# Kernel optimization log

Measured on AMD Instinct MI355X. Metric: run time of the kernel, lower is better.

Reference implementation:

```python
import jax, jax.numpy as jnp
import numpy as np

B, T, C = 2, 2048, 2048
H, HK = 16, 4
HD = C // H
N_REP = H // HK


def setup_inputs() -> dict:
    key = jax.random.key(0)
    ks = jax.random.split(key, 10)
    sc_in = 1.0 / np.sqrt(C)
    x = jax.random.normal(ks[0], (B, T, C), dtype=jnp.float32)
    # rotary embeddings (realistic cos/sin from inv_freq)
    inv_freq = 1.0 / (10000.0 ** (jnp.arange(0, HD, 2, dtype=jnp.float32) / HD))
    freqs = jnp.arange(T, dtype=jnp.float32)[:, None] * inv_freq[None, :]  # [T, HD/2]
    emb = jnp.concatenate([freqs, freqs], axis=-1)  # [T, HD]
    cos = jnp.broadcast_to(jnp.cos(emb)[None], (B, T, HD))
    sin = jnp.broadcast_to(jnp.sin(emb)[None], (B, T, HD))
    Wq = jax.random.normal(ks[1], (C, H * HD), dtype=jnp.float32) * sc_in
    bq = jnp.zeros((H * HD,), dtype=jnp.float32)
    Wk = jax.random.normal(ks[2], (C, HK * HD), dtype=jnp.float32) * sc_in
    bk = jnp.zeros((HK * HD,), dtype=jnp.float32)
    Wv = jax.random.normal(ks[3], (C, HK * HD), dtype=jnp.float32) * sc_in
    bv = jnp.zeros((HK * HD,), dtype=jnp.float32)
    Wo = jax.random.normal(ks[4], (C, C), dtype=jnp.float32) * sc_in
    return {"x": x, "cos": cos, "sin": sin, "Wq": Wq, "bq": bq,
            "Wk": Wk, "bk": bk, "Wv": Wv, "bv": bv, "Wo": Wo}


def _rotate_half(t):
    t1, t2 = jnp.split(t, 2, axis=-1)
    return jnp.concatenate([-t2, t1], axis=-1)


def reference(x, cos, sin, Wq, bq, Wk, bk, Wv, bv, Wo):
    b, t, c = x.shape
    q = (x @ Wq + bq).reshape(b, t, H, HD).transpose(0, 2, 1, 3)   # [B,H,T,HD]
    k = (x @ Wk + bk).reshape(b, t, HK, HD).transpose(0, 2, 1, 3)  # [B,HK,T,HD]
    v = (x @ Wv + bv).reshape(b, t, HK, HD).transpose(0, 2, 1, 3)  # [B,HK,T,HD]
    co = cos[:, None, :, :]  # [B,1,T,HD]
    si = sin[:, None, :, :]
    q = q * co + _rotate_half(q) * si
    k = k * co + _rotate_half(k) * si
    # GQA without materializing repeated K/V: group query heads per KV head
    qg = q.reshape(b, HK, N_REP, t, HD)
    scale = 1.0 / np.sqrt(HD)
    scores = jnp.einsum('bgrqd,bgkd->bgrqk', qg, k) * scale  # [B,HK,n_rep,T,T]
    causal = jnp.tril(jnp.ones((t, t), dtype=bool))
    scores = jnp.where(causal, scores, jnp.finfo(scores.dtype).min)
    att = jax.nn.softmax(scores, axis=-1)
    yg = jnp.einsum('bgrqk,bgkd->bgrqd', att, v)  # [B,HK,n_rep,T,HD]
    y = yg.reshape(b, H, t, HD).transpose(0, 2, 1, 3).reshape(b, t, c)
    return y @ Wo
```

## Files before the change

kernel.cpp:

```cpp
#include <hip/hip_runtime.h>
#include <math.h>

#define BB 2
#define TT 2048
#define CC 2048
#define HH 16
#define HKK 4
#define HD 128
#define MM (BB*TT)

typedef short bf16x8 __attribute__((ext_vector_type(8)));
typedef float f32x4 __attribute__((ext_vector_type(4)));

#define GLOBAL_AS(p) ((const __attribute__((address_space(1))) void*)(p))
#define LDS_AS(p)    ((__attribute__((address_space(3))) void*)(p))

__device__ __forceinline__ unsigned short f2bf(float f) {
    unsigned u = __float_as_uint(f);
    u += 0x7fff + ((u >> 16) & 1);
    return (unsigned short)(u >> 16);
}
__device__ __forceinline__ float bf2f(unsigned short h) {
    return __uint_as_float(((unsigned)h) << 16);
}

#define QSCALE (0.08838834764831845f * 1.44269504088896340736f)

__global__ __launch_bounds__(256) void cast_x_kernel(
    const float* __restrict__ x, unsigned short* __restrict__ xb)
{
    size_t i = ((size_t)blockIdx.x * 256 + threadIdx.x) * 8;
    float4 a = *(const float4*)&x[i];
    float4 b = *(const float4*)&x[i + 4];
    uint4 r;
    r.x = f2bf(a.x) | ((unsigned)f2bf(a.y) << 16);
    r.y = f2bf(a.z) | ((unsigned)f2bf(a.w) << 16);
    r.z = f2bf(b.x) | ((unsigned)f2bf(b.y) << 16);
    r.w = f2bf(b.z) | ((unsigned)f2bf(b.w) << 16);
    *(uint4*)&xb[i] = r;
}

__global__ __launch_bounds__(256) void wtrans_kernel(
    const float* __restrict__ Wq, const float* __restrict__ Wk,
    const float* __restrict__ Wv, const float* __restrict__ Wo,
    unsigned short* __restrict__ Wt, unsigned short* __restrict__ Wot)
{
    __shared__ float tile[64][65];
    int z = blockIdx.z;
    const float* src; unsigned short* dst; int ldW, nmax, noff;
    if (z == 0)      { src = Wq; dst = Wt;  ldW = 2048; nmax = 2048; noff = 0; }
    else if (z == 1) { src = Wk; dst = Wt;  ldW = 512;  nmax = 512;  noff = 2048; }
    else if (z == 2) { src = Wv; dst = Wt;  ldW = 512;  nmax = 512;  noff = 2560; }
    else             { src = Wo; dst = Wot; ldW = 2048; nmax = 2048; noff = 0; }
    int n0 = blockIdx.y * 64;
    if (n0 >= nmax) return;
    int k0 = blockIdx.x * 64;
    int tx = threadIdx.x & 15, ty = threadIdx.x >> 4;
#pragma unroll
    for (int i = 0; i < 4; ++i) {
        int r = ty + i * 16;
        float4 v4 = *(const float4*)&src[(size_t)(k0 + r) * ldW + n0 + tx * 4];
        tile[r][tx * 4 + 0] = v4.x;
        tile[r][tx * 4 + 1] = v4.y;
        tile[r][tx * 4 + 2] = v4.z;
        tile[r][tx * 4 + 3] = v4.w;
    }
    __syncthreads();
#pragma unroll
    for (int i = 0; i < 4; ++i) {
        int r = ty + i * 16;
        int c = tx * 4;
        ushort4 o;
        o.x = f2bf(tile[c + 0][r]);
        o.y = f2bf(tile[c + 1][r]);
        o.z = f2bf(tile[c + 2][r]);
        o.w = f2bf(tile[c + 3][r]);
        *(ushort4*)&dst[(size_t)(noff + n0 + r) * 2048 + k0 + c] = o;
    }
}

__device__ __forceinline__ void gemm_core_128x128x64(
    const unsigned short* __restrict__ A, const unsigned short* __restrict__ B,
    short* As, short* Bs, int m0, int n0,
    const int* mrow, const int* nrow, f32x4 (&acc)[4][4])
{
    const int tid = threadIdx.x;
    const int lane = tid & 63;
    const int w = tid >> 6;
    const int lm = lane & 15;
    const int q8 = lane >> 4;
    const int lrow = lane >> 3;
    const int lchunk = lane & 7;

    for (int kt = 0; kt < CC; kt += 64) {
        __syncthreads();
#pragma unroll
        for (int jj = 0; jj < 4; ++jj) {
            int rA = w * 32 + jj * 8 + lrow;
            int cA = ((lchunk ^ (rA & 7)) << 3);
            __builtin_amdgcn_global_load_lds(
                GLOBAL_AS(&A[(size_t)(m0 + rA) * CC + kt + cA]),
                LDS_AS(&As[(w * 32 + jj * 8) * 64]), 16, 0, 0);
            __builtin_amdgcn_global_load_lds(
                GLOBAL_AS(&B[(size_t)(n0 + rA) * CC + kt + cA]),
                LDS_AS(&Bs[(w * 32 + jj * 8) * 64]), 16, 0, 0);
        }
        __syncthreads();
#pragma unroll
        for (int ksi = 0; ksi < 2; ++ksi) {
            bf16x8 af[4], bfr[4];
#pragma unroll
            for (int i = 0; i < 4; ++i) {
                int xo = (((ksi * 4 + q8) ^ (lm & 7)) << 3);
                af[i]  = *(const bf16x8*)&As[(mrow[i] + lm) * 64 + xo];
                bfr[i] = *(const bf16x8*)&Bs[(nrow[i] + lm) * 64 + xo];
            }
#pragma unroll
            for (int im = 0; im < 4; ++im)
#pragma unroll
                for (int in = 0; in < 4; ++in)
                    acc[im][in] = __builtin_amdgcn_mfma_f32_16x16x32_bf16(af[im], bfr[in], acc[im][in], 0, 0, 0);
        }
    }
}

__global__ __launch_bounds__(256, 3) void qkv_gemm_mfma(
    const unsigned short* __restrict__ xb, const unsigned short* __restrict__ Wt,
    const float* __restrict__ bq, const float* __restrict__ bk, const float* __restrict__ bv,
    const float* __restrict__ cosb, const float* __restrict__ sinb,
    unsigned short* __restrict__ q, unsigned short* __restrict__ k, unsigned short* __restrict__ v)
{
    __shared__ __attribute__((aligned(16))) short As[128 * 64];
    __shared__ __attribute__((aligned(16))) short Bs[128 * 64];
    const int lane = threadIdx.x & 63;
    const int w = threadIdx.x >> 6;
    const int w1 = w >> 1;
    const int m0 = blockIdx.y * 128;
    const int n0 = blockIdx.x * 128;
    const int lm = lane & 15;
    const int q8 = lane >> 4;

    int mrow[4], nrow[4];
#pragma unroll
    for (int i = 0; i < 4; ++i) {
        mrow[i] = (w & 1) * 64 + i * 16;
        nrow[i] = w1 * 32 + (i & 1) * 16 + (i >> 1) * 64;
    }

    f32x4 acc[4][4];
#pragma unroll
    for (int im = 0; im < 4; ++im)
#pragma unroll
        for (int in = 0; in < 4; ++in) acc[im][in] = {0.f, 0.f, 0.f, 0.f};

    gemm_core_128x128x64(xb, Wt, As, Bs, m0, n0, mrow, nrow, acc);

    unsigned short* dst; const float* bias; int ldD, off, mode;
    if (n0 < 2048)      { dst = q; bias = bq; ldD = 2048; off = n0;        mode = 0; }
    else if (n0 < 2560) { dst = k; bias = bk; ldD = 512;  off = n0 - 2048; mode = 1; }
    else                { dst = v; bias = bv; ldD = 512;  off = n0 - 2560; mode = 2; }

    float bv_[4];
#pragma unroll
    for (int in = 0; in < 4; ++in) bv_[in] = bias[off + nrow[in] + lm];

#pragma unroll
    for (int im = 0; im < 4; ++im) {
        int rowbase = m0 + mrow[im] + q8 * 4;
        float t[4][4];
#pragma unroll
        for (int in = 0; in < 4; ++in)
#pragma unroll
            for (int r = 0; r < 4; ++r) t[in][r] = acc[im][in][r] + bv_[in];
        if (mode < 2) {
#pragma unroll
            for (int in = 0; in < 4; ++in) {
                int d = nrow[in] + lm;
                float sgn = (in < 2) ? -1.f : 1.f;
#pragma unroll
                for (int r = 0; r < 4; ++r) {
                    int row = rowbase + r;
                    float c = cosb[row * HD + d];
                    float s = sinb[row * HD + d];
                    float o = c * t[in][r] + sgn * s * t[in ^ 2][r];
                    if (mode == 0) o *= QSCALE;
                    dst[(size_t)row * ldD + off + d] = f2bf(o);
                }
            }
        } else {
#pragma unroll
            for (int in = 0; in < 4; ++in)
#pragma unroll
                for (int r = 0; r < 4; ++r)
                    dst[(size_t)(rowbase + r) * ldD + off + nrow[in] + lm] = f2bf(t[in][r]);
        }
    }
}

__global__ __launch_bounds__(256, 3) void out_gemm_mfma(
    const unsigned short* __restrict__ yb, const unsigned short* __restrict__ Wot,
    float* __restrict__ Cout)
{
    __shared__ __attribute__((aligned(16))) short As[128 * 64];
    __shared__ __attribute__((aligned(16))) short Bs[128 * 64];
    const int lane = threadIdx.x & 63;
    const int w = threadIdx.x >> 6;
    const int m0 = blockIdx.y * 128;
    const int n0 = blockIdx.x * 128;
    const int lm = lane & 15;
    const int q8 = lane >> 4;

    int mrow[4], nrow[4];
#pragma unroll
    for (int i = 0; i < 4; ++i) {
        mrow[i] = (w & 1) * 64 + i * 16;
        nrow[i] = (w >> 1) * 64 + i * 16;
    }

    f32x4 acc[4][4];
#pragma unroll
    for (int im = 0; im < 4; ++im)
#pragma unroll
        for (int in = 0; in < 4; ++in) acc[im][in] = {0.f, 0.f, 0.f, 0.f};

    gemm_core_128x128x64(yb, Wot, As, Bs, m0, n0, mrow, nrow, acc);

#pragma unroll
    for (int im = 0; im < 4; ++im)
#pragma unroll
        for (int in = 0; in < 4; ++in)
#pragma unroll
            for (int r = 0; r < 4; ++r) {
                int row = m0 + mrow[im] + q8 * 4 + r;
                Cout[(size_t)row * CC + n0 + nrow[in] + lm] = acc[im][in][r];
            }
}

__global__ __launch_bounds__(256) void vtrans_kernel(
    const unsigned short* __restrict__ v, unsigned short* __restrict__ vt)
{
    __shared__ unsigned short tile[64][68];
    int bg = blockIdx.z;
    int b = bg >> 2, g = bg & 3;
    int t0 = blockIdx.x * 64;
    int d0 = blockIdx.y * 64;
    int tx = threadIdx.x & 15, ty = threadIdx.x >> 4;
#pragma unroll
    for (int i = 0; i < 4; ++i) {
        int r = ty + i * 16;
        ushort4 v4 = *(const ushort4*)&v[(size_t)(b * TT + t0 + r) * (HKK * HD) + g * HD + d0 + tx * 4];
        tile[r][tx * 4 + 0] = v4.x;
        tile[r][tx * 4 + 1] = v4.y;
        tile[r][tx * 4 + 2] = v4.z;
        tile[r][tx * 4 + 3] = v4.w;
    }
    __syncthreads();
#pragma unroll
    for (int i = 0; i < 4; ++i) {
        int r = ty + i * 16;
        int c = tx * 4;
        ushort4 o;
        o.x = tile[c + 0][r];
        o.y = tile[c + 1][r];
        o.z = tile[c + 2][r];
        o.w = tile[c + 3][r];
        *(ushort4*)&vt[(size_t)(bg * HD + d0 + r) * TT + t0 + c] = o;
    }
}

__global__ __launch_bounds__(512, 4) void flash_mfma(
    const unsigned short* __restrict__ q, const unsigned short* __restrict__ k,
    const unsigned short* __restrict__ vt, unsigned short* __restrict__ y)
{
    __shared__ __attribute__((aligned(16))) short SM[27136];
    short* Ks = SM;
    short* Vs = SM + 8704;
    short* Ps = SM + 17920;

    const int tid = threadIdx.x;
    const int lane = tid & 63;
    const int w = tid >> 6;
    const int lm = lane & 15;
    const int q8 = lane >> 4;
    const int bh = blockIdx.x;
    const int b = bh >> 4, h = bh & 15, g = h >> 2;
    const int yb_ = blockIdx.y;
    const int qi = (yb_ < 8) ? (15 - yb_) : (yb_ - 8);
    const int q0 = qi * 128;
    const int wrow = w * 16;
    const int jdiag = 2 * qi + (w >> 2);
    const int jmax = 2 * qi + 1;

    bf16x8 qf[4];
#pragma unroll
    for (int ks = 0; ks < 4; ++ks)
        qf[ks] = *(const bf16x8*)&q[(size_t)(b * TT + q0 + wrow + lm) * CC
                                    + h * HD + ks * 32 + q8 * 8];

    f32x4 o_acc[8];
#pragma unroll
    for (int nt = 0; nt < 8; ++nt) o_acc[nt] = {0.f, 0.f, 0.f, 0.f};
    float m_i = -1e30f;
    float l_i = 0.f;

    int ktok[2], ke8[2], vd[2], vt8[2];
#pragma unroll
    for (int i = 0; i < 2; ++i) {
        int f = tid + i * 512;
        ktok[i] = f >> 4; ke8[i] = (f & 15) * 8;
        vd[i]   = f >> 3; vt8[i] = (f & 7) * 8;
    }
    const unsigned short* kbase = k + (size_t)(b * TT) * (HKK * HD) + g * HD;
    const unsigned short* vbase = vt + (size_t)((b * 4 + g) * HD) * TT;

    uint4 kreg[2], vreg[2];
#pragma unroll
    for (int i = 0; i < 2; ++i) {
        kreg[i] = *(const uint4*)&kbase[(size_t)ktok[i] * (HKK * HD) + ke8[i]];
        vreg[i] = *(const uint4*)&vbase[(size_t)vd[i] * TT + vt8[i]];
    }

    short* Pw = Ps + w * 16 * 72;
    const int mrow = (w & 3) * 16 + lm;

    for (int j = 0; j <= jmax; ++j) {
        __syncthreads();
#pragma unroll
        for (int i = 0; i < 2; ++i) {
            *(uint4*)&Ks[ktok[i] * 136 + ke8[i]] = kreg[i];
            *(uint4*)&Vs[vd[i] * 72 + vt8[i]]    = vreg[i];
        }
        __syncthreads();
        if (j < jmax) {
#pragma unroll
            for (int i = 0; i < 2; ++i) {
                kreg[i] = *(const uint4*)&kbase[(size_t)((j + 1) * 64 + ktok[i]) * (HKK * HD) + ke8[i]];
                vreg[i] = *(const uint4*)&vbase[(size_t)vd[i] * TT + (j + 1) * 64 + vt8[i]];
            }
        }

        if (j <= jdiag) {
            f32x4 sacc[4];
#pragma unroll
            for (int ct = 0; ct < 4; ++ct) {
                sacc[ct] = {0.f, 0.f, 0.f, 0.f};
#pragma unroll
                for (int ks = 0; ks < 4; ++ks) {
                    bf16x8 kf = *(const bf16x8*)&Ks[(ct * 16 + lm) * 136 + ks * 32 + q8 * 8];
                    sacc[ct] = __builtin_amdgcn_mfma_f32_16x16x32_bf16(kf, qf[ks], sacc[ct], 0, 0, 0);
                }
            }
            if (j == jdiag) {
#pragma unroll
                for (int ct = 0; ct < 4; ++ct)
#pragma unroll
                    for (int r = 0; r < 4; ++r)
                        if (ct * 16 + q8 * 4 + r > mrow) sacc[ct][r] = -1e30f;
            }
            float tmax = fmaxf(
                fmaxf(fmaxf(fmaxf(sacc[0][0], sacc[0][1]), fmaxf(sacc[0][2], sacc[0][3])),
                      fmaxf(fmaxf(sacc[1][0], sacc[1][1]), fmaxf(sacc[1][2], sacc[1][3]))),
                fmaxf(fmaxf(fmaxf(sacc[2][0], sacc[2][1]), fmaxf(sacc[2][2], sacc[2][3])),
                      fmaxf(fmaxf(sacc[3][0], sacc[3][1]), fmaxf(sacc[3][2], sacc[3][3]))));
            tmax = fmaxf(tmax, __shfl_xor(tmax, 16));
            tmax = fmaxf(tmax, __shfl_xor(tmax, 32));
            float m_new = fmaxf(m_i, tmax);
            float alpha = exp2f(m_i - m_new);
            m_i = m_new;

            float ps = 0.f;
#pragma unroll
            for (int ct = 0; ct < 4; ++ct) {
                ushort4 pp;
                float p0 = exp2f(sacc[ct][0] - m_new);
                float p1 = exp2f(sacc[ct][1] - m_new);
                float p2 = exp2f(sacc[ct][2] - m_new);
                float p3 = exp2f(sacc[ct][3] - m_new);
                ps += (p0 + p1) + (p2 + p3);
                pp.x = f2bf(p0); pp.y = f2bf(p1); pp.z = f2bf(p2); pp.w = f2bf(p3);
                *(ushort4*)&Pw[lm * 72 + ct * 16 + q8 * 4] = pp;
            }
            l_i = l_i * alpha + ps;

            float a0 = __shfl(alpha, q8 * 4 + 0);
            float a1 = __shfl(alpha, q8 * 4 + 1);
            float a2 = __shfl(alpha, q8 * 4 + 2);
            float a3 = __shfl(alpha, q8 * 4 + 3);
#pragma unroll
            for (int nt = 0; nt < 8; ++nt) {
                o_acc[nt][0] *= a0;
                o_acc[nt][1] *= a1;
                o_acc[nt][2] *= a2;
                o_acc[nt][3] *= a3;
            }

#pragma unroll
            for (int ks2 = 0; ks2 < 2; ++ks2) {
                bf16x8 pf = *(const bf16x8*)&Pw[lm * 72 + ks2 * 32 + q8 * 8];
#pragma unroll
                for (int nt = 0; nt < 8; ++nt) {
                    bf16x8 vf = *(const bf16x8*)&Vs[(nt * 16 + lm) * 72 + ks2 * 32 + q8 * 8];
                    o_acc[nt] = __builtin_amdgcn_mfma_f32_16x16x32_bf16(pf, vf, o_acc[nt], 0, 0, 0);
                }
            }
        }
    }

    float lf = l_i;
    lf += __shfl_xor(lf, 16);
    lf += __shfl_xor(lf, 32);
    float inv[4];
#pragma unroll
    for (int r = 0; r < 4; ++r) inv[r] = 1.f / __shfl(lf, q8 * 4 + r);

    __syncthreads();
    short* Es = SM;
#pragma unroll
    for (int nt = 0; nt < 8; ++nt)
#pragma unroll
        for (int r = 0; r < 4; ++r)
            Es[(w * 16 + q8 * 4 + r) * 136 + nt * 16 + lm] = (short)f2bf(o_acc[nt][r] * inv[r]);
    __syncthreads();
#pragma unroll
    for (int i = 0; i < 4; ++i) {
        int f = tid + i * 512;
        int row = f >> 4, ch = f & 15;
        uint4 t = *(const uint4*)&Es[row * 136 + ch * 8];
        *(uint4*)&y[(size_t)(b * TT + q0 + row) * CC + h * HD + ch * 8] = t;
    }
}

extern "C" void kernel_launch(void* const* d_in, const int* in_sizes, int n_in,
                              void* d_out, int out_size, void* d_ws, size_t ws_size,
                              hipStream_t stream) {
    const float* x    = (const float*)d_in[0];
    const float* cosb = (const float*)d_in[1];
    const float* sinb = (const float*)d_in[2];
    const float* Wq   = (const float*)d_in[3];
    const float* bq   = (const float*)d_in[4];
    const float* Wk   = (const float*)d_in[5];
    const float* bk   = (const float*)d_in[6];
    const float* Wv   = (const float*)d_in[7];
    const float* bv   = (const float*)d_in[8];
    const float* Wo   = (const float*)d_in[9];
    float* out = (float*)d_out;

    unsigned short* xb  = (unsigned short*)d_ws;
    unsigned short* Wt  = xb  + (size_t)MM * CC;
    unsigned short* Wot = Wt  + (size_t)3072 * 2048;
    unsigned short* qb  = Wot + (size_t)2048 * 2048;
    unsigned short* kb  = qb  + (size_t)MM * CC;
    unsigned short* vb  = kb  + (size_t)MM * (HKK * HD);
    unsigned short* vtb = vb  + (size_t)MM * (HKK * HD);
    unsigned short* ybf = vtb + (size_t)BB * HKK * HD * TT;

    cast_x_kernel<<<dim3((MM * CC) / 2048), 256, 0, stream>>>(x, xb);
    wtrans_kernel<<<dim3(32, 32, 4), 256, 0, stream>>>(Wq, Wk, Wv, Wo, Wt, Wot);
    qkv_gemm_mfma<<<dim3(3072 / 128, MM / 128), 256, 0, stream>>>(
        xb, Wt, bq, bk, bv, cosb, sinb, qb, kb, vb);
    vtrans_kernel<<<dim3(TT / 64, HD / 64, BB * HKK), 256, 0, stream>>>(vb, vtb);
    flash_mfma<<<dim3(BB * HH, TT / 128), 512, 0, stream>>>(qb, kb, vtb, ybf);
    out_gemm_mfma<<<dim3(CC / 128, MM / 128), 256, 0, stream>>>(ybf, Wot, out);
}
```

Baseline: 378.7 us.

## Split long causal query tiles across KV halves with a combine kernel

The attention grid grows from 16 to 24 query blocks per head. The eight longest causal query tiles (qi ≥ 8) are each split into two blocks that cover the first and second halves of the KV range, so per-block work is more even and the grid is larger. Split blocks write unnormalised-rescaled fp32 partial outputs and per-row softmax mass (l·2^m) into scratch, reusing d_out and the x-bf16 buffer. A new combine kernel merges each pair into the bf16 attention output. Launch bounds are also raised to 6 blocks per SM. The cost is an extra kernel and about 33 MB of fp32 partial traffic.

Measured after the change: 502.1 us. 1.33x slower.

```diff
diff --git a/kernel.cpp b/kernel.cpp
--- a/kernel.cpp
+++ b/kernel.cpp
@@ -268,9 +268,21 @@
     }
 }
 
-__global__ __launch_bounds__(512, 4) void flash_mfma(
+static __device__ const signed char QI_T[24] = {
+    15, 7, 14, 14, 13, 6, 12, 11,
+    15, 13, 12, 10, 10, 9, 11, 5,
+    0, 1, 2, 3, 8, 4, 8, 9
+};
+static __device__ const signed char HF_T[24] = {
+    0, 2, 0, 1, 1, 2, 1, 1,
+    1, 0, 0, 0, 1, 0, 0, 2,
+    2, 2, 2, 2, 0, 2, 1, 1
+};
+
+__global__ __launch_bounds__(512, 6) void flash_mfma(
     const unsigned short* __restrict__ q, const unsigned short* __restrict__ k,
-    const unsigned short* __restrict__ vt, unsigned short* __restrict__ y)
+    const unsigned short* __restrict__ vt, unsigned short* __restrict__ y,
+    float* __restrict__ po, float* __restrict__ sb)
 {
     __shared__ __attribute__((aligned(16))) short SM[27136];
     short* Ks = SM;
@@ -285,11 +297,15 @@
     const int bh = blockIdx.x;
     const int b = bh >> 4, h = bh & 15, g = h >> 2;
     const int yb_ = blockIdx.y;
-    const int qi = (yb_ < 8) ? (15 - yb_) : (yb_ - 8);
+    const int qi = QI_T[yb_];
+    const int hf = HF_T[yb_];
     const int q0 = qi * 128;
     const int wrow = w * 16;
     const int jdiag = 2 * qi + (w >> 2);
-    const int jmax = 2 * qi + 1;
+    int j0, jend;
+    if (hf == 2)      { j0 = 0;      jend = 2 * qi + 2; }
+    else if (hf == 0) { j0 = 0;      jend = qi + 1; }
+    else              { j0 = qi + 1; jend = 2 * qi + 2; }
 
     bf16x8 qf[4];
 #pragma unroll
@@ -316,14 +332,14 @@
     uint4 kreg[2], vreg[2];
 #pragma unroll
     for (int i = 0; i < 2; ++i) {
-        kreg[i] = *(const uint4*)&kbase[(size_t)ktok[i] * (HKK * HD) + ke8[i]];
-        vreg[i] = *(const uint4*)&vbase[(size_t)vd[i] * TT + vt8[i]];
+        kreg[i] = *(const uint4*)&kbase[(size_t)(j0 * 64 + ktok[i]) * (HKK * HD) + ke8[i]];
+        vreg[i] = *(const uint4*)&vbase[(size_t)vd[i] * TT + j0 * 64 + vt8[i]];
     }
 
     short* Pw = Ps + w * 16 * 72;
     const int mrow = (w & 3) * 16 + lm;
 
-    for (int j = 0; j <= jmax; ++j) {
+    for (int j = j0; j < jend; ++j) {
         __syncthreads();
 #pragma unroll
         for (int i = 0; i < 2; ++i) {
@@ -331,7 +347,7 @@
             *(uint4*)&Vs[vd[i] * 72 + vt8[i]]    = vreg[i];
         }
         __syncthreads();
-        if (j < jmax) {
+        if (j + 1 < jend) {
 #pragma unroll
             for (int i = 0; i < 2; ++i) {
                 kreg[i] = *(const uint4*)&kbase[(size_t)((j + 1) * 64 + ktok[i]) * (HKK * HD) + ke8[i]];
@@ -413,20 +429,61 @@
 #pragma unroll
     for (int r = 0; r < 4; ++r) inv[r] = 1.f / __shfl(lf, q8 * 4 + r);
 
-    __syncthreads();
-    short* Es = SM;
-#pragma unroll
-    for (int nt = 0; nt < 8; ++nt)
-#pragma unroll
-        for (int r = 0; r < 4; ++r)
-            Es[(w * 16 + q8 * 4 + r) * 136 + nt * 16 + lm] = (short)f2bf(o_acc[nt][r] * inv[r]);
-    __syncthreads();
-#pragma unroll
-    for (int i = 0; i < 4; ++i) {
-        int f = tid + i * 512;
-        int row = f >> 4, ch = f & 15;
-        uint4 t = *(const uint4*)&Es[row * 136 + ch * 8];
-        *(uint4*)&y[(size_t)(b * TT + q0 + row) * CC + h * HD + ch * 8] = t;
+    if (hf == 2) {
+        __syncthreads();
+        short* Es = SM;
+#pragma unroll
+        for (int nt = 0; nt < 8; ++nt)
+#pragma unroll
+            for (int r = 0; r < 4; ++r)
+                Es[(wrow + q8 * 4 + r) * 136 + nt * 16 + lm] = (short)f2bf(o_acc[nt][r] * inv[r]);
+        __syncthreads();
+#pragma unroll
+        for (int i = 0; i < 4; ++i) {
+            int f = tid + i * 512;
+            int row = f >> 4, ch = f & 15;
+            uint4 t = *(const uint4*)&Es[row * 136 + ch * 8];
+            *(uint4*)&y[(size_t)(b * TT + q0 + row) * CC + h * HD + ch * 8] = t;
+        }
+    } else {
+        const int pi = ((bh << 3) + (qi - 8)) * 2 + hf;
+        if (lane < 16) sb[pi * 128 + wrow + lane] = lf * exp2f(m_i);
+        float* pb = po + (size_t)pi * 16384;
+#pragma unroll
+        for (int nt = 0; nt < 8; ++nt)
+#pragma unroll
+            for (int r = 0; r < 4; ++r)
+                pb[(wrow + q8 * 4 + r) * 128 + nt * 16 + lm] = o_acc[nt][r] * inv[r];
+    }
+}
+
+__global__ __launch_bounds__(256) void combine_kernel(
+    const float* __restrict__ po, const float* __restrict__ sb,
+    unsigned short* __restrict__ y)
+{
+    const int bh = blockIdx.x;
+    const int b = bh >> 4, h = bh & 15;
+    const int qi = 8 + blockIdx.y;
+    const int p0 = ((bh << 3) + (qi - 8)) * 2;
+    const int t = threadIdx.x;
+    const int row = t >> 1, d0 = (t & 1) * 64;
+    float s0 = sb[p0 * 128 + row];
+    float s1 = sb[(p0 + 1) * 128 + row];
+    float w0 = s0 / (s0 + s1);
+    float w1 = 1.f - w0;
+    const float* a = &po[(size_t)p0 * 16384 + row * 128 + d0];
+    const float* c = &po[(size_t)(p0 + 1) * 16384 + row * 128 + d0];
+    unsigned short* yr = &y[(size_t)(b * TT + qi * 128 + row) * CC + h * HD + d0];
+#pragma unroll
+    for (int i = 0; i < 64; i += 4) {
+        float4 xa = *(const float4*)&a[i];
+        float4 xc = *(const float4*)&c[i];
+        ushort4 o;
+        o.x = f2bf(w0 * xa.x + w1 * xc.x);
+        o.y = f2bf(w0 * xa.y + w1 * xc.y);
+        o.z = f2bf(w0 * xa.z + w1 * xc.z);
+        o.w = f2bf(w0 * xa.w + w1 * xc.w);
+        *(ushort4*)&yr[i] = o;
     }
 }
 
@@ -454,11 +511,15 @@
     unsigned short* vtb = vb  + (size_t)MM * (HKK * HD);
     unsigned short* ybf = vtb + (size_t)BB * HKK * HD * TT;
 
+    float* po = (float*)d_out;
+    float* sbuf = (float*)xb;
+
     cast_x_kernel<<<dim3((MM * CC) / 2048), 256, 0, stream>>>(x, xb);
     wtrans_kernel<<<dim3(32, 32, 4), 256, 0, stream>>>(Wq, Wk, Wv, Wo, Wt, Wot);
     qkv_gemm_mfma<<<dim3(3072 / 128, MM / 128), 256, 0, stream>>>(
         xb, Wt, bq, bk, bv, cosb, sinb, qb, kb, vb);
     vtrans_kernel<<<dim3(TT / 64, HD / 64, BB * HKK), 256, 0, stream>>>(vb, vtb);
-    flash_mfma<<<dim3(BB * HH, TT / 128), 512, 0, stream>>>(qb, kb, vtb, ybf);
+    flash_mfma<<<dim3(BB * HH, 24), 512, 0, stream>>>(qb, kb, vtb, ybf, po, sbuf);
+    combine_kernel<<<dim3(BB * HH, 8), 256, 0, stream>>>(po, sbuf, ybf);
     out_gemm_mfma<<<dim3(CC / 128, MM / 128), 256, 0, stream>>>(ybf, Wot, out);
 }
```
